# Kernel optimization log

Measured on AMD Instinct MI355X. Metric: run time of the kernel, lower is better.

Reference implementation:

```python
import jax, jax.numpy as jnp
import numpy as np

NUM_HEADS = 2
LN_EPS = 1e-5


def setup_inputs() -> dict:
    key = jax.random.key(0)
    ks = jax.random.split(key, 4)
    bs, C, H, W = 32, 512, 64, 64
    T, token_dim = 64, 128
    features = jax.random.normal(ks[0], (bs, C, H, W), dtype=jnp.float32)
    tokens = jax.random.normal(ks[1], (T, bs, token_dim), dtype=jnp.float32)
    q_w = jax.random.normal(ks[2], (C, token_dim), dtype=jnp.float32) * (token_dim ** -0.5)
    q_b = jnp.zeros((C,), dtype=jnp.float32)
    proj_w = jax.random.normal(ks[3], (token_dim, C), dtype=jnp.float32) * (C ** -0.5)
    proj_b = jnp.zeros((token_dim,), dtype=jnp.float32)
    ln_w = jnp.ones((token_dim,), dtype=jnp.float32)
    ln_b = jnp.zeros((token_dim,), dtype=jnp.float32)
    return {"features": features, "tokens": tokens, "q_w": q_w, "q_b": q_b,
            "proj_w": proj_w, "proj_b": proj_b, "ln_w": ln_w, "ln_b": ln_b}


def reference(features, tokens, q_w, q_b, proj_w, proj_b, ln_w, ln_b):
    bs, C, H, W = features.shape
    T = tokens.shape[0]
    nh = NUM_HEADS
    ch = C // nh
    scale = ch ** -0.5
    # q projection: [T, bs, token_dim] -> [T, bs, C] -> [bs, nh, T, ch]
    t = (tokens @ q_w.T + q_b).reshape(T, bs, nh, ch).transpose(1, 2, 0, 3)
    # keys (reused as values): [bs, nh, ch, H*W]
    k = features.reshape(bs, nh, ch, H * W)
    # attention scores over spatial positions
    attn = jnp.einsum('bhtc,bhcs->bhts', t, k) * scale  # [bs, nh, T, HW]
    a = jax.nn.softmax(attn, axis=-1)
    attn_out = jnp.einsum('bhts,bhcs->bhtc', a, k)      # [bs, nh, T, ch]
    # back to [T, bs, C], project, residual, layernorm
    t_a = attn_out.transpose(2, 0, 1, 3).reshape(T, bs, C)
    t_a = t_a @ proj_w.T + proj_b
    tok = tokens + t_a
    mu = jnp.mean(tok, axis=-1, keepdims=True)
    var = jnp.var(tok, axis=-1, keepdims=True)
    tok = (tok - mu) * jax.lax.rsqrt(var + LN_EPS) * ln_w + ln_b
    return tok, attn.reshape(bs, nh, T, H, W)
```

## Files before the change

kernel.cpp:

```cpp
#include <hip/hip_runtime.h>
#include <stdint.h>
#include <stddef.h>

typedef __attribute__((ext_vector_type(8))) __bf16 bf16x8;
typedef __attribute__((ext_vector_type(4))) __bf16 bf16x4;
typedef __attribute__((ext_vector_type(4))) float f32x4;

#define NC 8
#define SCHUNK 512
#define SS 32
#define NSUB 16
#define KNW 40

__global__ __launch_bounds__(128) void k_qproj(
    const float* __restrict__ tokens, const float* __restrict__ q_w,
    const float* __restrict__ q_b, __bf16* __restrict__ ws_q)
{
    const int t = blockIdx.x >> 3;
    const int b0 = (blockIdx.x & 7) * 4;
    const int d = threadIdx.x;
    __shared__ float tok[4][128];
    #pragma unroll
    for (int j = 0; j < 4; ++j)
        tok[j][d] = tokens[((size_t)t * 32 + b0 + j) * 128 + d];
    __syncthreads();
    #pragma unroll
    for (int i = 0; i < 4; ++i) {
        const int c = d + 128 * i;
        const float* wr = q_w + (size_t)c * 128;
        const float qb = q_b[c];
        float acc[4] = {qb, qb, qb, qb};
        #pragma unroll 4
        for (int k = 0; k < 128; k += 4) {
            const float4 w4 = *(const float4*)(wr + k);
            #pragma unroll
            for (int j = 0; j < 4; ++j) {
                const float4 t4 = *(const float4*)&tok[j][k];
                acc[j] += t4.x * w4.x + t4.y * w4.y + t4.z * w4.z + t4.w * w4.w;
            }
        }
        const int h = c >> 8, cc = c & 255;
        #pragma unroll
        for (int j = 0; j < 4; ++j)
            ws_q[(size_t)(((b0 + j) * 2 + h) * 64 + t) * 256 + cc] = (__bf16)acc[j];
    }
}

__global__ __launch_bounds__(256, 2) void k_attn(
    const float* __restrict__ feat, const __bf16* __restrict__ ws_q,
    float* __restrict__ attn_g, float* __restrict__ part, float* __restrict__ zbuf)
{
    const int bh = blockIdx.x >> 3;
    const int nc = blockIdx.x & 7;
    const int b = bh >> 1, h = bh & 1;
    const int tid = threadIdx.x;
    const int lane = tid & 63;
    const int w = tid >> 6;
    const int l15 = lane & 15, g = lane >> 4;
    const int t0 = w * 16;

    __shared__ __bf16 kT[SS * 256];
    __shared__ __bf16 knat[256 * KNW];
    __shared__ __bf16 P[64 * KNW];

    bf16x8 afr[8];
    {
        const __bf16* qb = ws_q + ((size_t)bh * 64 + t0 + l15) * 256 + g * 8;
        #pragma unroll
        for (int kk = 0; kk < 8; ++kk)
            afr[kk] = *(const bf16x8*)(qb + kk * 32);
    }

    f32x4 acc[16];
    #pragma unroll
    for (int i = 0; i < 16; ++i) { acc[i][0]=0.f; acc[i][1]=0.f; acc[i][2]=0.f; acc[i][3]=0.f; }
    float zp[4] = {0.f, 0.f, 0.f, 0.f};

    const float* fb = feat + ((size_t)b * 512 + (size_t)h * 256) * 4096;
    const int sw_base = nc * SCHUNK;
    const int s4 = (tid & 7) * 4;
    const int c0 = tid >> 3;
    const float* fptr = fb + (size_t)c0 * 4096 + sw_base + s4;

    float4 f4[8];
    #pragma unroll
    for (int p = 0; p < 8; ++p)
        f4[p] = *(const float4*)(fptr + (size_t)p * 32 * 4096);

    #pragma unroll 1
    for (int ss = 0; ss < NSUB; ++ss) {
        __syncthreads();
        #pragma unroll
        for (int p = 0; p < 8; ++p) {
            const int c = c0 + p * 32;
            bf16x4 nb;
            nb[0] = (__bf16)f4[p].x; nb[1] = (__bf16)f4[p].y;
            nb[2] = (__bf16)f4[p].z; nb[3] = (__bf16)f4[p].w;
            *(bf16x4*)&knat[c * KNW + s4] = nb;
            kT[(s4+0) * 256 + (c ^ (((s4+0) & 15) << 3))] = nb[0];
            kT[(s4+1) * 256 + (c ^ (((s4+1) & 15) << 3))] = nb[1];
            kT[(s4+2) * 256 + (c ^ (((s4+2) & 15) << 3))] = nb[2];
            kT[(s4+3) * 256 + (c ^ (((s4+3) & 15) << 3))] = nb[3];
        }
        __syncthreads();
        if (ss < NSUB - 1) {
            #pragma unroll
            for (int p = 0; p < 8; ++p)
                f4[p] = *(const float4*)(fptr + (ss + 1) * SS + (size_t)p * 32 * 4096);
        }
        const int sw = sw_base + ss * SS;
        #pragma unroll
        for (int nt = 0; nt < 2; ++nt) {
            f32x4 d; d[0]=0.f; d[1]=0.f; d[2]=0.f; d[3]=0.f;
            #pragma unroll
            for (int kk = 0; kk < 8; ++kk) {
                const int cc = kk * 32 + g * 8;
                const bf16x8 bfr = *(bf16x8*)&kT[(nt * 16 + l15) * 256 + (cc ^ (l15 << 3))];
                d = __builtin_amdgcn_mfma_f32_16x16x32_bf16(afr[kk], bfr, d, 0, 0, 0);
            }
            #pragma unroll
            for (int r = 0; r < 4; ++r) {
                const int t = t0 + g * 4 + r;
                const float sv = d[r] * 0.0625f;
                attn_g[((size_t)bh * 64 + t) * 4096 + sw + nt * 16 + l15] = sv;
                const float p = __expf(sv);
                zp[r] += p;
                P[t * KNW + nt * 16 + l15] = (__bf16)p;
            }
        }
        const bf16x8 pa = *(bf16x8*)&P[(t0 + l15) * KNW + g * 8];
        #pragma unroll
        for (int ct = 0; ct < 16; ++ct) {
            const bf16x8 kb = *(bf16x8*)&knat[(ct * 16 + l15) * KNW + g * 8];
            acc[ct] = __builtin_amdgcn_mfma_f32_16x16x32_bf16(pa, kb, acc[ct], 0, 0, 0);
        }
    }

    const size_t pbase = (size_t)(bh * NC + nc) * 64 * 256;
    #pragma unroll
    for (int ct = 0; ct < 16; ++ct)
        #pragma unroll
        for (int r = 0; r < 4; ++r)
            part[pbase + (size_t)(t0 + g * 4 + r) * 256 + ct * 16 + l15] = acc[ct][r];
    #pragma unroll
    for (int r = 0; r < 4; ++r) {
        float z = zp[r];
        z += __shfl_xor(z, 1); z += __shfl_xor(z, 2);
        z += __shfl_xor(z, 4); z += __shfl_xor(z, 8);
        if (l15 == 0) zbuf[(size_t)(bh * NC + nc) * 64 + t0 + g * 4 + r] = z;
    }
}

__global__ __launch_bounds__(128) void k_post(
    const float* __restrict__ tokens, const float* __restrict__ proj_w,
    const float* __restrict__ proj_b, const float* __restrict__ ln_w,
    const float* __restrict__ ln_b, const float* __restrict__ part,
    const float* __restrict__ zbuf, float* __restrict__ out_tok)
{
    const int t = blockIdx.x >> 3;
    const int b0 = (blockIdx.x & 7) * 4;
    const int d = threadIdx.x;
    __shared__ float av[4][512];
    __shared__ float Zs[4][2];
    __shared__ float red[2][4][2];

    #pragma unroll
    for (int bb = 0; bb < 4; ++bb) {
        const int b = b0 + bb;
        #pragma unroll
        for (int i = 0; i < 4; ++i) {
            const int c = d + 128 * i;
            const int bh = b * 2 + (c >> 8), cc = c & 255;
            float s = 0.f;
            #pragma unroll
            for (int nc = 0; nc < NC; ++nc)
                s += part[((size_t)(bh * NC + nc) * 64 + t) * 256 + cc];
            av[bb][c] = s;
        }
    }
    if (d < 8) {
        const int bb = d >> 1, hh = d & 1;
        const int bh = (b0 + bb) * 2 + hh;
        float z = 0.f;
        for (int nc = 0; nc < NC; ++nc) z += zbuf[(size_t)(bh * NC + nc) * 64 + t];
        Zs[bb][hh] = z;
    }
    __syncthreads();
    #pragma unroll
    for (int bb = 0; bb < 4; ++bb) {
        const float rz0 = 1.f / Zs[bb][0], rz1 = 1.f / Zs[bb][1];
        #pragma unroll
        for (int i = 0; i < 4; ++i) {
            const int c = d + 128 * i;
            av[bb][c] *= (c < 256) ? rz0 : rz1;
        }
    }
    __syncthreads();

    const float pb = proj_b[d];
    float acc4[4] = {pb, pb, pb, pb};
    const float* wr = proj_w + (size_t)d * 512;
    #pragma unroll 4
    for (int k = 0; k < 512; k += 4) {
        const float4 w4 = *(const float4*)(wr + k);
        #pragma unroll
        for (int bb = 0; bb < 4; ++bb) {
            const float4 a4 = *(const float4*)&av[bb][k];
            acc4[bb] += a4.x * w4.x + a4.y * w4.y + a4.z * w4.z + a4.w * w4.w;
        }
    }
    float r[4], s1[4], s2[4];
    #pragma unroll
    for (int bb = 0; bb < 4; ++bb) {
        r[bb] = tokens[((size_t)t * 32 + b0 + bb) * 128 + d] + acc4[bb];
        s1[bb] = r[bb]; s2[bb] = r[bb] * r[bb];
    }
    #pragma unroll
    for (int o = 1; o < 64; o <<= 1)
        #pragma unroll
        for (int bb = 0; bb < 4; ++bb) {
            s1[bb] += __shfl_xor(s1[bb], o);
            s2[bb] += __shfl_xor(s2[bb], o);
        }
    const int wv = d >> 6;
    if ((d & 63) == 0)
        #pragma unroll
        for (int bb = 0; bb < 4; ++bb) { red[0][bb][wv] = s1[bb]; red[1][bb][wv] = s2[bb]; }
    __syncthreads();
    #pragma unroll
    for (int bb = 0; bb < 4; ++bb) {
        const float mean = (red[0][bb][0] + red[0][bb][1]) * (1.f / 128.f);
        const float ex2  = (red[1][bb][0] + red[1][bb][1]) * (1.f / 128.f);
        const float var = ex2 - mean * mean;
        out_tok[((size_t)t * 32 + b0 + bb) * 128 + d] =
            (r[bb] - mean) * rsqrtf(var + 1e-5f) * ln_w[d] + ln_b[d];
    }
}

extern "C" void kernel_launch(void* const* d_in, const int* in_sizes, int n_in,
                              void* d_out, int out_size, void* d_ws, size_t ws_size,
                              hipStream_t stream) {
    const float* features = (const float*)d_in[0];
    const float* tokens   = (const float*)d_in[1];
    const float* q_w      = (const float*)d_in[2];
    const float* q_b      = (const float*)d_in[3];
    const float* proj_w   = (const float*)d_in[4];
    const float* proj_b   = (const float*)d_in[5];
    const float* ln_w     = (const float*)d_in[6];
    const float* ln_b     = (const float*)d_in[7];

    float* out = (float*)d_out;
    float* out_attn = out + (size_t)64 * 32 * 128;

    __bf16* ws_q = (__bf16*)d_ws;
    float* part = (float*)((char*)d_ws + (size_t)2 * 1024 * 1024);
    float* zbuf = part + (size_t)64 * NC * 64 * 256;

    k_qproj<<<512, 128, 0, stream>>>(tokens, q_w, q_b, ws_q);
    k_attn<<<64 * NC, 256, 0, stream>>>(features, ws_q, out_attn, part, zbuf);
    k_post<<<512, 128, 0, stream>>>(tokens, proj_w, proj_b, ln_w, ln_b, part, zbuf, out);
}
```

Before: 138.0 us.

## Keep feature tiles in registers for PV MFMA and drop native-layout LDS copy

The feature load pattern now matches the MFMA B-operand layout, so each thread keeps its converted bf16 key fragment in registers (kreg) and uses it directly for the P·K product. This removes the knat shared-memory buffer and its writes and reads. The output accumulation is repartitioned so each wave owns 64 channels across all 64 tokens rather than 16 tokens across all channels. The P·K step for a sub-chunk is deferred to the start of the next iteration, with a tail step after the loop, to stay within the existing barriers. In exchange, kT is written with scalar bf16 stores, and the wave-to-wave dependency on P forces all waves to read every P row.

```diff
diff --git a/kernel.cpp b/kernel.cpp
--- a/kernel.cpp
+++ b/kernel.cpp
@@ -3,14 +3,16 @@
 #include <stddef.h>
 
 typedef __attribute__((ext_vector_type(8))) __bf16 bf16x8;
-typedef __attribute__((ext_vector_type(4))) __bf16 bf16x4;
 typedef __attribute__((ext_vector_type(4))) float f32x4;
 
 #define NC 8
 #define SCHUNK 512
 #define SS 32
 #define NSUB 16
-#define KNW 40
+#define KTP 256
+#define PP 40
+
+#define MFMA __builtin_amdgcn_mfma_f32_16x16x32_bf16
 
 __global__ __launch_bounds__(128) void k_qproj(
     const float* __restrict__ tokens, const float* __restrict__ q_w,
@@ -59,9 +61,8 @@
     const int l15 = lane & 15, g = lane >> 4;
     const int t0 = w * 16;
 
-    __shared__ __bf16 kT[SS * 256];
-    __shared__ __bf16 knat[256 * KNW];
-    __shared__ __bf16 P[64 * KNW];
+    __shared__ __bf16 kT[SS * KTP];
+    __shared__ __bf16 P[64 * PP];
 
     bf16x8 afr[8];
     {
@@ -76,47 +77,62 @@
     for (int i = 0; i < 16; ++i) { acc[i][0]=0.f; acc[i][1]=0.f; acc[i][2]=0.f; acc[i][3]=0.f; }
     float zp[4] = {0.f, 0.f, 0.f, 0.f};
 
-    const float* fb = feat + ((size_t)b * 512 + (size_t)h * 256) * 4096;
-    const int sw_base = nc * SCHUNK;
-    const int s4 = (tid & 7) * 4;
-    const int c0 = tid >> 3;
-    const float* fptr = fb + (size_t)c0 * 4096 + sw_base + s4;
+    const float* fsrc = feat + ((size_t)b * 512 + (size_t)h * 256) * 4096
+                      + (size_t)(w * 64 + l15) * 4096 + nc * SCHUNK + g * 8;
 
     float4 f4[8];
     #pragma unroll
-    for (int p = 0; p < 8; ++p)
-        f4[p] = *(const float4*)(fptr + (size_t)p * 32 * 4096);
+    for (int ct = 0; ct < 4; ++ct) {
+        f4[2*ct]   = *(const float4*)(fsrc + (size_t)ct * 16 * 4096);
+        f4[2*ct+1] = *(const float4*)(fsrc + (size_t)ct * 16 * 4096 + 4);
+    }
+
+    bf16x8 kreg[4];
 
     #pragma unroll 1
     for (int ss = 0; ss < NSUB; ++ss) {
         __syncthreads();
-        #pragma unroll
-        for (int p = 0; p < 8; ++p) {
-            const int c = c0 + p * 32;
-            bf16x4 nb;
-            nb[0] = (__bf16)f4[p].x; nb[1] = (__bf16)f4[p].y;
-            nb[2] = (__bf16)f4[p].z; nb[3] = (__bf16)f4[p].w;
-            *(bf16x4*)&knat[c * KNW + s4] = nb;
-            kT[(s4+0) * 256 + (c ^ (((s4+0) & 15) << 3))] = nb[0];
-            kT[(s4+1) * 256 + (c ^ (((s4+1) & 15) << 3))] = nb[1];
-            kT[(s4+2) * 256 + (c ^ (((s4+2) & 15) << 3))] = nb[2];
-            kT[(s4+3) * 256 + (c ^ (((s4+3) & 15) << 3))] = nb[3];
+        if (ss > 0) {
+            #pragma unroll
+            for (int tt = 0; tt < 4; ++tt) {
+                const bf16x8 pa = *(const bf16x8*)&P[(tt * 16 + l15) * PP + g * 8];
+                #pragma unroll
+                for (int ct = 0; ct < 4; ++ct)
+                    acc[tt * 4 + ct] = MFMA(pa, kreg[ct], acc[tt * 4 + ct], 0, 0, 0);
+            }
+        }
+        #pragma unroll
+        for (int ct = 0; ct < 4; ++ct) {
+            const float4 a = f4[2*ct], c4 = f4[2*ct+1];
+            bf16x8 kv;
+            kv[0]=(__bf16)a.x;  kv[1]=(__bf16)a.y;  kv[2]=(__bf16)a.z;  kv[3]=(__bf16)a.w;
+            kv[4]=(__bf16)c4.x; kv[5]=(__bf16)c4.y; kv[6]=(__bf16)c4.z; kv[7]=(__bf16)c4.w;
+            kreg[ct] = kv;
+            const int c = w * 64 + ct * 16 + l15;
+            #pragma unroll
+            for (int j = 0; j < 8; ++j) {
+                const int s = g * 8 + j;
+                kT[s * KTP + (c ^ ((s & 15) << 3))] = kv[j];
+            }
+        }
+        if (ss < NSUB - 1) {
+            const float* p2 = fsrc + (ss + 1) * SS;
+            #pragma unroll
+            for (int ct = 0; ct < 4; ++ct) {
+                f4[2*ct]   = *(const float4*)(p2 + (size_t)ct * 16 * 4096);
+                f4[2*ct+1] = *(const float4*)(p2 + (size_t)ct * 16 * 4096 + 4);
+            }
         }
         __syncthreads();
-        if (ss < NSUB - 1) {
-            #pragma unroll
-            for (int p = 0; p < 8; ++p)
-                f4[p] = *(const float4*)(fptr + (ss + 1) * SS + (size_t)p * 32 * 4096);
-        }
-        const int sw = sw_base + ss * SS;
+        const int sw = nc * SCHUNK + ss * SS;
         #pragma unroll
         for (int nt = 0; nt < 2; ++nt) {
             f32x4 d; d[0]=0.f; d[1]=0.f; d[2]=0.f; d[3]=0.f;
             #pragma unroll
             for (int kk = 0; kk < 8; ++kk) {
                 const int cc = kk * 32 + g * 8;
-                const bf16x8 bfr = *(bf16x8*)&kT[(nt * 16 + l15) * 256 + (cc ^ (l15 << 3))];
-                d = __builtin_amdgcn_mfma_f32_16x16x32_bf16(afr[kk], bfr, d, 0, 0, 0);
+                const bf16x8 bfr = *(const bf16x8*)&kT[(nt * 16 + l15) * KTP + (cc ^ (l15 << 3))];
+                d = MFMA(afr[kk], bfr, d, 0, 0, 0);
             }
             #pragma unroll
             for (int r = 0; r < 4; ++r) {
@@ -125,23 +141,28 @@
                 attn_g[((size_t)bh * 64 + t) * 4096 + sw + nt * 16 + l15] = sv;
                 const float p = __expf(sv);
                 zp[r] += p;
-                P[t * KNW + nt * 16 + l15] = (__bf16)p;
-            }
-        }
-        const bf16x8 pa = *(bf16x8*)&P[(t0 + l15) * KNW + g * 8];
-        #pragma unroll
-        for (int ct = 0; ct < 16; ++ct) {
-            const bf16x8 kb = *(bf16x8*)&knat[(ct * 16 + l15) * KNW + g * 8];
-            acc[ct] = __builtin_amdgcn_mfma_f32_16x16x32_bf16(pa, kb, acc[ct], 0, 0, 0);
-        }
+                P[t * PP + nt * 16 + l15] = (__bf16)p;
+            }
+        }
+    }
+    __syncthreads();
+    #pragma unroll
+    for (int tt = 0; tt < 4; ++tt) {
+        const bf16x8 pa = *(const bf16x8*)&P[(tt * 16 + l15) * PP + g * 8];
+        #pragma unroll
+        for (int ct = 0; ct < 4; ++ct)
+            acc[tt * 4 + ct] = MFMA(pa, kreg[ct], acc[tt * 4 + ct], 0, 0, 0);
     }
 
     const size_t pbase = (size_t)(bh * NC + nc) * 64 * 256;
     #pragma unroll
-    for (int ct = 0; ct < 16; ++ct)
-        #pragma unroll
-        for (int r = 0; r < 4; ++r)
-            part[pbase + (size_t)(t0 + g * 4 + r) * 256 + ct * 16 + l15] = acc[ct][r];
+    for (int tt = 0; tt < 4; ++tt)
+        #pragma unroll
+        for (int ct = 0; ct < 4; ++ct)
+            #pragma unroll
+            for (int r = 0; r < 4; ++r)
+                part[pbase + (size_t)(tt * 16 + g * 4 + r) * 256 + w * 64 + ct * 16 + l15]
+                    = acc[tt * 4 + ct][r];
     #pragma unroll
     for (int r = 0; r < 4; ++r) {
         float z = zp[r];
```

Result: no change. 138.2 us (+0.2%).
